# Optimization experiments

Measured on AMD Instinct MI355X. Metric: run time of the kernel, lower is better.

The kernel has to match this reference:

```python
import jax, jax.numpy as jnp
import numpy as np

N_HEADS = 16
HEAD_DIM = 64
HIDDEN = N_HEADS * HEAD_DIM


def setup_inputs() -> dict:
    key = jax.random.key(0)
    ks = jax.random.split(key, 10)
    B, F, T = 2, 2048, 2048
    std = 0.02
    inp = {
        "from_tensor": jax.random.normal(ks[0], (B, F, HIDDEN), dtype=jnp.float32),
        "to_tensor": jax.random.normal(ks[1], (B, T, HIDDEN), dtype=jnp.float32),
        "attention_mask": jax.random.randint(ks[2], (B, F, T), 0, 2, dtype=jnp.int32),
        "Wq": jax.random.normal(ks[3], (HIDDEN, HIDDEN), dtype=jnp.float32) * std,
        "bq": jnp.zeros((HIDDEN,), dtype=jnp.float32),
        "Wk": jax.random.normal(ks[4], (HIDDEN, HIDDEN), dtype=jnp.float32) * std,
        "bk": jnp.zeros((HIDDEN,), dtype=jnp.float32),
        "Wv": jax.random.normal(ks[5], (HIDDEN, HIDDEN), dtype=jnp.float32) * std,
        "bv": jnp.zeros((HIDDEN,), dtype=jnp.float32),
    }
    return inp


def reference(from_tensor, to_tensor, attention_mask, Wq, bq, Wk, bk, Wv, bv):
    B, F, _ = from_tensor.shape
    T = to_tensor.shape[1]
    N, H = N_HEADS, HEAD_DIM

    # QKV projections (no activations: query/key/value act fns are None)
    q = (from_tensor @ Wq + bq).reshape(B, F, N, H)
    k = (to_tensor @ Wk + bk).reshape(B, T, N, H)
    v = (to_tensor @ Wv + bv).reshape(B, T, N, H)

    scores = jnp.einsum('BFNH,BTNH->BNFT', q, k) * (1.0 / np.sqrt(float(H)))
    # additive mask: mask [B,F,T] -> [B,1,F,T]; 0 entries get -10000
    adder = (1.0 - attention_mask.astype(jnp.float32))[:, None, :, :] * -10000.0
    scores = scores + adder
    probs = jax.nn.softmax(scores, axis=-1)  # dropout skipped (inference)

    context = jnp.einsum('BNFT,BTNH->BFNH', probs, v)
    return context.reshape(B, F, N * H)
```

## Files before the change

kernel.cpp:

```cpp
#include <hip/hip_runtime.h>


typedef short v8s __attribute__((ext_vector_type(8)));
typedef float v4f __attribute__((ext_vector_type(4)));
typedef unsigned short u16;
typedef unsigned int   u32;
typedef unsigned long long u64;

constexpr float QSCALE = 0.18033688011112042f;

__device__ __forceinline__ u16 f2bf(float f) {
    u32 u = __builtin_bit_cast(u32, f);
    u += 0x7fffu + ((u >> 16) & 1u);
    return (u16)(u >> 16);
}

__device__ __forceinline__ u32 pack_trunc(float a, float b) {
    u32 ua = __builtin_bit_cast(u32, a);
    u32 ub = __builtin_bit_cast(u32, b);
    return (ua >> 16) | (ub & 0xffff0000u);
}

__device__ __forceinline__ v8s ld8(const u16* p) {
    return *reinterpret_cast<const v8s*>(p);
}

__device__ __forceinline__ void async16(const void* g, void* l) {
    __builtin_amdgcn_global_load_lds(
        (const __attribute__((address_space(1))) u32*)g,
        (__attribute__((address_space(3))) u32*)l, 16, 0, 0);
}

__global__ void cvt_bf16(const float* __restrict__ src, u16* __restrict__ dst, int n4) {
    int i = blockIdx.x * blockDim.x + threadIdx.x;
    if (i < n4) {
        float4 v = reinterpret_cast<const float4*>(src)[i];
        ushort4 o;
        o.x = f2bf(v.x); o.y = f2bf(v.y); o.z = f2bf(v.z); o.w = f2bf(v.w);
        reinterpret_cast<ushort4*>(dst)[i] = o;
    }
}

__global__ void transpose_w(const float* __restrict__ Wq, const float* __restrict__ Wk,
                            const float* __restrict__ Wv,
                            u16* __restrict__ Wqt, u16* __restrict__ Wkt, u16* __restrict__ Wvt) {
    __shared__ float tile[32][33];
    const float* W = blockIdx.z == 0 ? Wq : (blockIdx.z == 1 ? Wk : Wv);
    u16* Wt = blockIdx.z == 0 ? Wqt : (blockIdx.z == 1 ? Wkt : Wvt);
    const int tx = threadIdx.x, ty = threadIdx.y;
    const int n0 = blockIdx.x * 32, k0 = blockIdx.y * 32;
    for (int i = 0; i < 4; i++)
        tile[ty + i * 8][tx] = W[(size_t)(k0 + ty + i * 8) * 1024 + n0 + tx];
    __syncthreads();
    for (int i = 0; i < 4; i++)
        Wt[(size_t)(n0 + ty + i * 8) * 1024 + k0 + tx] = f2bf(tile[tx][ty + i * 8]);
}

__global__ void mask_pack(const int* __restrict__ mask, u64* __restrict__ words, int nwords) {
    int g = blockIdx.x * blockDim.x + threadIdx.x;
    int w = g >> 6, lane = g & 63;
    if (w < nwords) {
        int v = mask[(size_t)w * 64 + lane];
        u64 bits = __ballot(v != 0);
        if (lane == 0) words[w] = bits;
    }
}

__global__ __launch_bounds__(256) void gemm_qkv(
    const u16* __restrict__ Xf, const u16* __restrict__ Xt,
    const u16* __restrict__ Wqt, const u16* __restrict__ Wkt, const u16* __restrict__ Wvt,
    const float* __restrict__ bq, const float* __restrict__ bk, const float* __restrict__ bv,
    u16* __restrict__ Qb, u16* __restrict__ Kb, u16* __restrict__ Vtb) {
    const int z = blockIdx.z;
    const u16* A      = z == 0 ? Xf : Xt;
    const u16* Bt     = z == 0 ? Wqt : (z == 1 ? Wkt : Wvt);
    const float* bias = z == 0 ? bq : (z == 1 ? bk : bv);
    u16* C            = z == 0 ? Qb : (z == 1 ? Kb : Vtb);
    const int mode    = (z == 2);
    const float sc    = (z == 0) ? QSCALE : 1.0f;

    __shared__ u16 As[128 * 32];
    __shared__ u16 Bs[128 * 32];
    const uint4* Ag = reinterpret_cast<const uint4*>(A);
    const uint4* Bg = reinterpret_cast<const uint4*>(Bt);

    const int tid = threadIdx.x;
    const int lane = tid & 63, wave = tid >> 6;
    const int quad = lane >> 4, l16 = lane & 15;
    const int wm = wave >> 1, wn = wave & 1;
    const int m0 = blockIdx.x * 128, n0 = blockIdx.y * 128;

    const int cg  = (lane & 3) ^ ((lane >> 3) & 3);
    const int sw8 = (quad ^ ((l16 >> 1) & 3)) * 8;

    const int r0 = (wave * 2 + 0) * 16 + (lane >> 2);
    const int r1 = (wave * 2 + 1) * 16 + (lane >> 2);
    const uint4* ap0 = Ag + (size_t)(m0 + r0) * 128 + cg;
    const uint4* ap1 = Ag + (size_t)(m0 + r1) * 128 + cg;
    const uint4* bp0 = Bg + (size_t)(n0 + r0) * 128 + cg;
    const uint4* bp1 = Bg + (size_t)(n0 + r1) * 128 + cg;

    v4f acc[4][4];
    for (int i = 0; i < 4; i++)
        for (int j = 0; j < 4; j++) acc[i][j] = (v4f)0.0f;

    for (int k0 = 0; k0 < 32; k0++) {
        __syncthreads();
        async16(ap0, As + (wave * 2 + 0) * 512); ap0 += 4;
        async16(ap1, As + (wave * 2 + 1) * 512); ap1 += 4;
        async16(bp0, Bs + (wave * 2 + 0) * 512); bp0 += 4;
        async16(bp1, Bs + (wave * 2 + 1) * 512); bp1 += 4;
        __syncthreads();

        v8s af[4], bf[4];
        #pragma unroll
        for (int mt = 0; mt < 4; mt++) af[mt] = ld8(&As[(wm * 64 + mt * 16 + l16) * 32 + sw8]);
        #pragma unroll
        for (int nt = 0; nt < 4; nt++) bf[nt] = ld8(&Bs[(wn * 64 + nt * 16 + l16) * 32 + sw8]);
        #pragma unroll
        for (int mt = 0; mt < 4; mt++)
            #pragma unroll
            for (int nt = 0; nt < 4; nt++)
                acc[mt][nt] = __builtin_amdgcn_mfma_f32_16x16x32_bf16(af[mt], bf[nt], acc[mt][nt], 0, 0, 0);
    }

    #pragma unroll
    for (int nt = 0; nt < 4; nt++) {
        const int col = n0 + wn * 64 + nt * 16 + l16;
        const float bv = bias[col];
        #pragma unroll
        for (int mt = 0; mt < 4; mt++) {
            const int mbase = m0 + wm * 64 + mt * 16 + quad * 4;
            if (mode == 0) {
                for (int r = 0; r < 4; r++)
                    C[(size_t)(mbase + r) * 1024 + col] = f2bf((acc[mt][nt][r] + bv) * sc);
            } else {
                const int b = mbase >> 11, t = mbase & 2047;
                const int head = col >> 6, h = col & 63;
                ushort4 pk;
                pk.x = f2bf(acc[mt][nt][0] + bv);
                pk.y = f2bf(acc[mt][nt][1] + bv);
                pk.z = f2bf(acc[mt][nt][2] + bv);
                pk.w = f2bf(acc[mt][nt][3] + bv);
                *reinterpret_cast<ushort4*>(&C[(size_t)((b * 16 + head) * 64 + h) * 2048 + t]) = pk;
            }
        }
    }
}

__global__ __launch_bounds__(256, 2) void attn_fused(
    const u16* __restrict__ Qb, const u16* __restrict__ Kb,
    const u16* __restrict__ Vtb, const u64* __restrict__ mw,
    float* __restrict__ out) {
    __shared__ u16 Qs[2][128][32];
    __shared__ u16 Ks[2][64][32];
    __shared__ u16 Vs[2][64][32];
    __shared__ u32 Ps[4][32 * 36];

    const int tid = threadIdx.x;
    const int lane = tid & 63, wave = tid >> 6;
    const int quad = lane >> 4, l16 = lane & 15;
    const int b = blockIdx.x >> 4, head = blockIdx.x & 15;
    const int f0 = blockIdx.y * 128;

    const uint4* Qg = reinterpret_cast<const uint4*>(Qb);
    const uint4* Kg = reinterpret_cast<const uint4*>(Kb);
    const uint4* Vg = reinterpret_cast<const uint4*>(Vtb);
    const size_t vbase4 = (size_t)(b * 16 + head) * 64 * 256;

    const int cg  = (lane & 3) ^ ((lane >> 3) & 3);
    const int sw8 = (quad ^ ((l16 >> 1) & 3)) * 8;

    #pragma unroll
    for (int j = 0; j < 4; j++) {
        const int d = (wave * 4 + j) * 64 + lane;
        const int row = d >> 2, half = row >> 7, q = row & 127;
        async16(Qg + (((size_t)(b * 2048 + f0 + q) * 16 + head) * 8 + half * 4 + cg),
                (u16*)Qs + (wave * 4 + j) * 512);
    }

    const int kr0 = ((wave * 2 + 0) * 64 + lane) >> 2;
    const int kr1 = ((wave * 2 + 1) * 64 + lane) >> 2;
    const uint4* kp0 = Kg + ((size_t)(b * 2048 + (kr0 & 63)) * 16 + head) * 8 + (kr0 >> 6) * 4 + cg;
    const uint4* kp1 = Kg + ((size_t)(b * 2048 + (kr1 & 63)) * 16 + head) * 8 + (kr1 >> 6) * 4 + cg;
    const uint4* vp0 = Vg + vbase4 + (size_t)(kr0 & 63) * 256 + (kr0 >> 6) * 4 + cg;
    const uint4* vp1 = Vg + vbase4 + (size_t)(kr1 & 63) * 256 + (kr1 >> 6) * 4 + cg;

    float lsum[2] = {0.f, 0.f};
    v4f accO[2][4];
    #pragma unroll
    for (int qh = 0; qh < 2; qh++)
        for (int ht = 0; ht < 4; ht++) accO[qh][ht] = (v4f)0.0f;

    u32* myPs = Ps[wave];
    const u64* mrow = mw + (size_t)(b * 2048 + f0 + wave * 32 + l16) * 32;

    for (int it = 0; it < 32; it++) {
        __syncthreads();
        async16(kp0, (u16*)Ks + (wave * 2 + 0) * 512); kp0 += 8192;
        async16(kp1, (u16*)Ks + (wave * 2 + 1) * 512); kp1 += 8192;
        async16(vp0, (u16*)Vs + (wave * 2 + 0) * 512); vp0 += 8;
        async16(vp1, (u16*)Vs + (wave * 2 + 1) * 512); vp1 += 8;
        __syncthreads();

        v4f s[2][4];
        #pragma unroll
        for (int qh = 0; qh < 2; qh++)
            for (int mt = 0; mt < 4; mt++) s[qh][mt] = (v4f)0.0f;
        #pragma unroll
        for (int kk = 0; kk < 2; kk++) {
            v8s kf[4];
            #pragma unroll
            for (int mt = 0; mt < 4; mt++) kf[mt] = ld8(&Ks[kk][mt * 16 + l16][sw8]);
            #pragma unroll
            for (int qh = 0; qh < 2; qh++) {
                v8s qf = ld8(&Qs[kk][wave * 32 + qh * 16 + l16][sw8]);
                #pragma unroll
                for (int mt = 0; mt < 4; mt++)
                    s[qh][mt] = __builtin_amdgcn_mfma_f32_16x16x32_bf16(kf[mt], qf, s[qh][mt], 0, 0, 0);
            }
        }

        u32 pk[2][8];
        #pragma unroll
        for (int qh = 0; qh < 2; qh++) {
            const u64 w = mrow[qh * 512 + it];
            const u32 lo = (u32)(w >> (quad * 4));
            const u32 hi = (u32)(w >> (quad * 4 + 32));
            float sum = 0.f;
            #pragma unroll
            for (int mt = 0; mt < 4; mt++) {
                const u32 bits = ((mt & 2) ? hi : lo) >> ((mt & 1) * 16);
                float p[4];
                #pragma unroll
                for (int r = 0; r < 4; r++) {
                    const float e = __builtin_amdgcn_exp2f(s[qh][mt][r]);
                    p[r] = ((bits >> r) & 1u) ? e : 0.0f;
                    sum += p[r];
                }
                pk[qh][mt * 2]     = pack_trunc(p[0], p[1]);
                pk[qh][mt * 2 + 1] = pack_trunc(p[2], p[3]);
            }
            lsum[qh] += sum;
        }

        #pragma unroll
        for (int qh = 0; qh < 2; qh++) {
            const int row = qh * 16 + l16;
            #pragma unroll
            for (int mt = 0; mt < 4; mt++)
                *reinterpret_cast<uint2*>(&myPs[row * 36 + mt * 8 + quad * 2]) =
                    make_uint2(pk[qh][mt * 2], pk[qh][mt * 2 + 1]);
        }

        #pragma unroll
        for (int kk = 0; kk < 2; kk++) {
            v8s vf[4];
            #pragma unroll
            for (int ht = 0; ht < 4; ht++) vf[ht] = ld8(&Vs[kk][ht * 16 + l16][sw8]);
            #pragma unroll
            for (int qh = 0; qh < 2; qh++) {
                const v8s pf = *reinterpret_cast<const v8s*>(
                    &myPs[(qh * 16 + l16) * 36 + kk * 16 + quad * 4]);
                #pragma unroll
                for (int ht = 0; ht < 4; ht++)
                    accO[qh][ht] = __builtin_amdgcn_mfma_f32_16x16x32_bf16(vf[ht], pf, accO[qh][ht], 0, 0, 0);
            }
        }
    }

    #pragma unroll
    for (int qh = 0; qh < 2; qh++) {
        float l = lsum[qh];
        l += __shfl_xor(l, 16);
        l += __shfl_xor(l, 32);
        const float inv = 1.0f / l;
        const size_t ro = (size_t)(b * 2048 + f0 + wave * 32 + qh * 16 + l16) * 1024 + head * 64;
        #pragma unroll
        for (int ht = 0; ht < 4; ht++) {
            float4 o;
            o.x = accO[qh][ht][0] * inv;
            o.y = accO[qh][ht][1] * inv;
            o.z = accO[qh][ht][2] * inv;
            o.w = accO[qh][ht][3] * inv;
            *reinterpret_cast<float4*>(&out[ro + ht * 16 + quad * 4]) = o;
        }
    }
}

extern "C" void kernel_launch(void* const* d_in, const int* in_sizes, int n_in,
                              void* d_out, int out_size, void* d_ws, size_t ws_size,
                              hipStream_t stream) {
    const float* from = (const float*)d_in[0];
    const float* to   = (const float*)d_in[1];
    const int*   mask = (const int*)d_in[2];
    const float* Wq = (const float*)d_in[3];
    const float* bq = (const float*)d_in[4];
    const float* Wk = (const float*)d_in[5];
    const float* bk = (const float*)d_in[6];
    const float* Wv = (const float*)d_in[7];
    const float* bv = (const float*)d_in[8];
    float* out = (float*)d_out;

    u16* Xf  = (u16*)d_ws;
    u16* Xt  = Xf  + 4194304;
    u16* Wqt = Xt  + 4194304;
    u16* Wkt = Wqt + 1048576;
    u16* Wvt = Wkt + 1048576;
    u16* Qb  = Wvt + 1048576;
    u16* Kb  = Qb  + 4194304;
    u16* Vtb = Kb  + 4194304;
    u64* mwords = (u64*)(Vtb + 4194304);

    cvt_bf16<<<4096, 256, 0, stream>>>(from, Xf, 1048576);
    cvt_bf16<<<4096, 256, 0, stream>>>(to, Xt, 1048576);
    transpose_w<<<dim3(32, 32, 3), dim3(32, 8), 0, stream>>>(Wq, Wk, Wv, Wqt, Wkt, Wvt);
    mask_pack<<<32768, 256, 0, stream>>>(mask, mwords, 131072);

    gemm_qkv<<<dim3(32, 8, 3), 256, 0, stream>>>(Xf, Xt, Wqt, Wkt, Wvt, bq, bk, bv, Qb, Kb, Vtb);

    attn_fused<<<dim3(32, 16), 256, 0, stream>>>(Qb, Kb, Vtb, mwords, out);
}
```

Before: 243.6 us.

## Double-buffer K/V tiles in attention, keep Q in registers, merge conversion kernels

The attention loop now prefetches the next K/V tile into a second LDS buffer while the current tile is computed. This replaces two barriers per iteration with one and hides global-to-LDS load latency. Q fragments are loaded once into registers instead of staged through LDS, and the two fp32-to-bf16 conversion launches are merged into one. The probability packing switches from truncation to round-to-nearest, which adds a few ALU ops per element, and the extra registers and LDS could lower occupancy.

```diff
diff --git a/kernel.cpp b/kernel.cpp
--- a/kernel.cpp
+++ b/kernel.cpp
@@ -15,9 +15,11 @@
     return (u16)(u >> 16);
 }
 
-__device__ __forceinline__ u32 pack_trunc(float a, float b) {
+__device__ __forceinline__ u32 pack_bf16(float a, float b) {
     u32 ua = __builtin_bit_cast(u32, a);
     u32 ub = __builtin_bit_cast(u32, b);
+    ua += 0x7fffu + ((ua >> 16) & 1u);
+    ub += 0x7fffu + ((ub >> 16) & 1u);
     return (ua >> 16) | (ub & 0xffff0000u);
 }
 
@@ -31,14 +33,18 @@
         (__attribute__((address_space(3))) u32*)l, 16, 0, 0);
 }
 
-__global__ void cvt_bf16(const float* __restrict__ src, u16* __restrict__ dst, int n4) {
+__global__ void cvt_bf16_2(const float* __restrict__ a, const float* __restrict__ bsrc,
+                           u16* __restrict__ da, u16* __restrict__ db, int n4) {
     int i = blockIdx.x * blockDim.x + threadIdx.x;
-    if (i < n4) {
-        float4 v = reinterpret_cast<const float4*>(src)[i];
-        ushort4 o;
-        o.x = f2bf(v.x); o.y = f2bf(v.y); o.z = f2bf(v.z); o.w = f2bf(v.w);
-        reinterpret_cast<ushort4*>(dst)[i] = o;
-    }
+    const float4* s;
+    ushort4* d;
+    int j;
+    if (i < n4) { s = (const float4*)a;    d = (ushort4*)da; j = i; }
+    else        { s = (const float4*)bsrc; d = (ushort4*)db; j = i - n4; }
+    float4 v = s[j];
+    ushort4 o;
+    o.x = f2bf(v.x); o.y = f2bf(v.y); o.z = f2bf(v.z); o.w = f2bf(v.w);
+    d[j] = o;
 }
 
 __global__ void transpose_w(const float* __restrict__ Wq, const float* __restrict__ Wk,
@@ -127,21 +133,21 @@
     #pragma unroll
     for (int nt = 0; nt < 4; nt++) {
         const int col = n0 + wn * 64 + nt * 16 + l16;
-        const float bv = bias[col];
+        const float bvv = bias[col];
         #pragma unroll
         for (int mt = 0; mt < 4; mt++) {
             const int mbase = m0 + wm * 64 + mt * 16 + quad * 4;
             if (mode == 0) {
                 for (int r = 0; r < 4; r++)
-                    C[(size_t)(mbase + r) * 1024 + col] = f2bf((acc[mt][nt][r] + bv) * sc);
+                    C[(size_t)(mbase + r) * 1024 + col] = f2bf((acc[mt][nt][r] + bvv) * sc);
             } else {
                 const int b = mbase >> 11, t = mbase & 2047;
                 const int head = col >> 6, h = col & 63;
                 ushort4 pk;
-                pk.x = f2bf(acc[mt][nt][0] + bv);
-                pk.y = f2bf(acc[mt][nt][1] + bv);
-                pk.z = f2bf(acc[mt][nt][2] + bv);
-                pk.w = f2bf(acc[mt][nt][3] + bv);
+                pk.x = f2bf(acc[mt][nt][0] + bvv);
+                pk.y = f2bf(acc[mt][nt][1] + bvv);
+                pk.z = f2bf(acc[mt][nt][2] + bvv);
+                pk.w = f2bf(acc[mt][nt][3] + bvv);
                 *reinterpret_cast<ushort4*>(&C[(size_t)((b * 16 + head) * 64 + h) * 2048 + t]) = pk;
             }
         }
@@ -152,9 +158,8 @@
     const u16* __restrict__ Qb, const u16* __restrict__ Kb,
     const u16* __restrict__ Vtb, const u64* __restrict__ mw,
     float* __restrict__ out) {
-    __shared__ u16 Qs[2][128][32];
-    __shared__ u16 Ks[2][64][32];
-    __shared__ u16 Vs[2][64][32];
+    __shared__ u16 Ks[2][2][64][32];
+    __shared__ u16 Vs[2][2][64][32];
     __shared__ u32 Ps[4][32 * 36];
 
     const int tid = threadIdx.x;
@@ -163,7 +168,6 @@
     const int b = blockIdx.x >> 4, head = blockIdx.x & 15;
     const int f0 = blockIdx.y * 128;
 
-    const uint4* Qg = reinterpret_cast<const uint4*>(Qb);
     const uint4* Kg = reinterpret_cast<const uint4*>(Kb);
     const uint4* Vg = reinterpret_cast<const uint4*>(Vtb);
     const size_t vbase4 = (size_t)(b * 16 + head) * 64 * 256;
@@ -171,13 +175,13 @@
     const int cg  = (lane & 3) ^ ((lane >> 3) & 3);
     const int sw8 = (quad ^ ((l16 >> 1) & 3)) * 8;
 
+    v8s qf[2][2];
     #pragma unroll
-    for (int j = 0; j < 4; j++) {
-        const int d = (wave * 4 + j) * 64 + lane;
-        const int row = d >> 2, half = row >> 7, q = row & 127;
-        async16(Qg + (((size_t)(b * 2048 + f0 + q) * 16 + head) * 8 + half * 4 + cg),
-                (u16*)Qs + (wave * 4 + j) * 512);
-    }
+    for (int kk = 0; kk < 2; kk++)
+        #pragma unroll
+        for (int qh = 0; qh < 2; qh++)
+            qf[kk][qh] = ld8(Qb + ((size_t)(b * 2048 + f0 + wave * 32 + qh * 16 + l16) * 16 + head) * 64
+                                + kk * 32 + quad * 8);
 
     const int kr0 = ((wave * 2 + 0) * 64 + lane) >> 2;
     const int kr1 = ((wave * 2 + 1) * 64 + lane) >> 2;
@@ -185,6 +189,7 @@
     const uint4* kp1 = Kg + ((size_t)(b * 2048 + (kr1 & 63)) * 16 + head) * 8 + (kr1 >> 6) * 4 + cg;
     const uint4* vp0 = Vg + vbase4 + (size_t)(kr0 & 63) * 256 + (kr0 >> 6) * 4 + cg;
     const uint4* vp1 = Vg + vbase4 + (size_t)(kr1 & 63) * 256 + (kr1 >> 6) * 4 + cg;
+    const int dK0 = (wave * 2 + 0) * 512, dK1 = (wave * 2 + 1) * 512;
 
     float lsum[2] = {0.f, 0.f};
     v4f accO[2][4];
@@ -195,13 +200,20 @@
     u32* myPs = Ps[wave];
     const u64* mrow = mw + (size_t)(b * 2048 + f0 + wave * 32 + l16) * 32;
 
+    async16(kp0, (u16*)Ks + dK0); kp0 += 8192;
+    async16(kp1, (u16*)Ks + dK1); kp1 += 8192;
+    async16(vp0, (u16*)Vs + dK0); vp0 += 8;
+    async16(vp1, (u16*)Vs + dK1); vp1 += 8;
+    __syncthreads();
+
     for (int it = 0; it < 32; it++) {
-        __syncthreads();
-        async16(kp0, (u16*)Ks + (wave * 2 + 0) * 512); kp0 += 8192;
-        async16(kp1, (u16*)Ks + (wave * 2 + 1) * 512); kp1 += 8192;
-        async16(vp0, (u16*)Vs + (wave * 2 + 0) * 512); vp0 += 8;
-        async16(vp1, (u16*)Vs + (wave * 2 + 1) * 512); vp1 += 8;
-        __syncthreads();
+        const int cur = it & 1, nxt = cur ^ 1;
+        if (it < 31) {
+            async16(kp0, (u16*)Ks + nxt * 4096 + dK0); kp0 += 8192;
+            async16(kp1, (u16*)Ks + nxt * 4096 + dK1); kp1 += 8192;
+            async16(vp0, (u16*)Vs + nxt * 4096 + dK0); vp0 += 8;
+            async16(vp1, (u16*)Vs + nxt * 4096 + dK1); vp1 += 8;
+        }
 
         v4f s[2][4];
         #pragma unroll
@@ -211,14 +223,12 @@
         for (int kk = 0; kk < 2; kk++) {
             v8s kf[4];
             #pragma unroll
-            for (int mt = 0; mt < 4; mt++) kf[mt] = ld8(&Ks[kk][mt * 16 + l16][sw8]);
-            #pragma unroll
-            for (int qh = 0; qh < 2; qh++) {
-                v8s qf = ld8(&Qs[kk][wave * 32 + qh * 16 + l16][sw8]);
+            for (int mt = 0; mt < 4; mt++) kf[mt] = ld8(&Ks[cur][kk][mt * 16 + l16][sw8]);
+            #pragma unroll
+            for (int qh = 0; qh < 2; qh++)
                 #pragma unroll
                 for (int mt = 0; mt < 4; mt++)
-                    s[qh][mt] = __builtin_amdgcn_mfma_f32_16x16x32_bf16(kf[mt], qf, s[qh][mt], 0, 0, 0);
-            }
+                    s[qh][mt] = __builtin_amdgcn_mfma_f32_16x16x32_bf16(kf[mt], qf[kk][qh], s[qh][mt], 0, 0, 0);
         }
 
         u32 pk[2][8];
@@ -238,8 +248,8 @@
                     p[r] = ((bits >> r) & 1u) ? e : 0.0f;
                     sum += p[r];
                 }
-                pk[qh][mt * 2]     = pack_trunc(p[0], p[1]);
-                pk[qh][mt * 2 + 1] = pack_trunc(p[2], p[3]);
+                pk[qh][mt * 2]     = pack_bf16(p[0], p[1]);
+                pk[qh][mt * 2 + 1] = pack_bf16(p[2], p[3]);
             }
             lsum[qh] += sum;
         }
@@ -257,7 +267,7 @@
         for (int kk = 0; kk < 2; kk++) {
             v8s vf[4];
             #pragma unroll
-            for (int ht = 0; ht < 4; ht++) vf[ht] = ld8(&Vs[kk][ht * 16 + l16][sw8]);
+            for (int ht = 0; ht < 4; ht++) vf[ht] = ld8(&Vs[cur][kk][ht * 16 + l16][sw8]);
             #pragma unroll
             for (int qh = 0; qh < 2; qh++) {
                 const v8s pf = *reinterpret_cast<const v8s*>(
@@ -267,6 +277,8 @@
                     accO[qh][ht] = __builtin_amdgcn_mfma_f32_16x16x32_bf16(vf[ht], pf, accO[qh][ht], 0, 0, 0);
             }
         }
+
+        __syncthreads();
     }
 
     #pragma unroll
@@ -312,8 +324,7 @@
     u16* Vtb = Kb  + 4194304;
     u64* mwords = (u64*)(Vtb + 4194304);
 
-    cvt_bf16<<<4096, 256, 0, stream>>>(from, Xf, 1048576);
-    cvt_bf16<<<4096, 256, 0, stream>>>(to, Xt, 1048576);
+    cvt_bf16_2<<<8192, 256, 0, stream>>>(from, to, Xf, Xt, 1048576);
     transpose_w<<<dim3(32, 32, 3), dim3(32, 8), 0, stream>>>(Wq, Wk, Wv, Wqt, Wkt, Wvt);
     mask_pack<<<32768, 256, 0, stream>>>(mask, mwords, 131072);
 
```

Result: slower. 251.6 us (+3.3%).
